# Kernel tuning notes

Measured on AMD Instinct MI355X. Metric: run time of the kernel, lower is better.

## Reference

```python
import jax, jax.numpy as jnp
import numpy as np

B, CIN, COUT, N = 64, 1024, 1024, 49   # batch, in_features, out_features, flattened spatial
GROUPS = 1
CHUNK = 16                              # output-channel tile to bound intermediate memory


def setup_inputs() -> dict:
    key = jax.random.key(0)
    k1, k2 = jax.random.split(key)
    x = jax.random.normal(k1, (B, CIN, N), dtype=jnp.float32)
    weight = jax.random.normal(k2, (COUT, CIN // GROUPS), dtype=jnp.float32)  # std=1.0 init
    bias = jnp.zeros((COUT,), dtype=jnp.float32)
    return {"x": x, "weight": weight, "bias": bias}


def norm_dist_inf(x, weight, groups, chunk):
    # x: [B, Cin, N], weight: [Cout, Cin//groups]
    # out[b, o, n] = max_d |x[b, g(o)*d + d', n] - weight[o, d']|  (L-inf distance)
    Bb, Cin, Nn = x.shape
    Cout, d = weight.shape
    og = Cout // groups
    xg = x.reshape(Bb, groups, d, Nn)                 # [B, g, d, N]
    wg = weight.reshape(groups, og, d)                # [g, og, d]
    # tile output channels to avoid materializing [B, Cout, Cin, N]
    wchunks = wg.reshape(groups, og // chunk, chunk, d).transpose(1, 0, 2, 3)  # [nc, g, chunk, d]

    def body(carry, wc):
        # diff: [B, g, chunk, d, N] -> max over d
        out = jnp.max(jnp.abs(xg[:, :, None, :, :] - wc[None, :, :, :, None]), axis=3)
        return carry, out                              # [B, g, chunk, N]

    _, outs = jax.lax.scan(body, None, wchunks)        # [nc, B, g, chunk, N]
    out = outs.transpose(1, 2, 0, 3, 4).reshape(Bb, Cout, Nn)
    return out


def reference(x, weight, bias):
    out = norm_dist_inf(x, weight, GROUPS, CHUNK)      # [B, Cout, N]
    return out + bias[None, :, None]
```

## Files before the change

### kernel.cpp

```cpp
#include <hip/hip_runtime.h>


constexpr int CIN  = 1024;
constexpr int COUT = 1024;
constexpr int NN   = 49;
constexpr int BB   = 64;
constexpr int P    = BB * NN;
constexpr int CPW  = 8;
constexpr int WPB  = 4;
constexpr int CPB  = CPW * WPB;
constexpr int KU   = 8;

__global__ __launch_bounds__(256) void ndist_kernel(
    const float* __restrict__ x, const float* __restrict__ w,
    const float* __restrict__ bias, float* __restrict__ out)
{
    const int lane = threadIdx.x & 63;
    const int wid  = __builtin_amdgcn_readfirstlane(threadIdx.x >> 6);

    const int p = blockIdx.x * BB + lane;
    const int b = p / NN;
    const int n = p - b * NN;
    const int o0 = blockIdx.y * CPB + wid * CPW;

    const float* __restrict__ xrow = x + (size_t)b * CIN * NN + n;

    float acc[CPW];
#pragma unroll
    for (int c = 0; c < CPW; ++c) acc[c] = 0.0f;

    for (int k0 = 0; k0 < CIN; k0 += KU) {
        float xv[KU];
#pragma unroll
        for (int j = 0; j < KU; ++j) xv[j] = xrow[(k0 + j) * NN];

#pragma unroll
        for (int c = 0; c < CPW; ++c) {
            const float* __restrict__ wr = w + (size_t)(o0 + c) * CIN + k0;
#pragma unroll
            for (int j = 0; j < KU; j += 2) {
                float d0 = xv[j]     - wr[j];
                float d1 = xv[j + 1] - wr[j + 1];
                acc[c] = fmaxf(fmaxf(acc[c], __builtin_fabsf(d0)),
                               __builtin_fabsf(d1));
            }
        }
    }

#pragma unroll
    for (int c = 0; c < CPW; ++c) {
        const int o = o0 + c;
        out[((size_t)b * COUT + o) * NN + n] = acc[c] + bias[o];
    }
}

extern "C" void kernel_launch(void* const* d_in, const int* in_sizes, int n_in,
                              void* d_out, int out_size, void* d_ws, size_t ws_size,
                              hipStream_t stream) {
    const float* x    = (const float*)d_in[0];
    const float* w    = (const float*)d_in[1];
    const float* bias = (const float*)d_in[2];
    float* out        = (float*)d_out;

    dim3 grid(P / BB, COUT / CPB);
    ndist_kernel<<<grid, 256, 0, stream>>>(x, w, bias, out);
}
```

Measured before the change: 150.8 us.

## Repack weights and use packed f32 subtract with max3 for L-inf distance

Adds a pre-pass that reorders weights into a k-tile by channel-group layout, so each wave reads a contiguous scalar block of 8 channels by 4 k values. The inner loop uses inline-asm v_pk_add_f32 with an SGPR weight operand to compute two channel differences per instruction, and v_max3_f32 with abs modifiers to fold two differences into the accumulator. It also double-buffers the x loads across k-tiles. This cuts VALU instruction count per element, at the cost of an extra 4 MB weight repack kernel on every call and a dependence on workspace size, with a fallback path when the workspace is too small.

```diff
diff --git a/kernel.cpp b/kernel.cpp
--- a/kernel.cpp
+++ b/kernel.cpp
@@ -1,5 +1,7 @@
 #include <hip/hip_runtime.h>
 
+
+typedef float v2f __attribute__((ext_vector_type(2)));
 
 constexpr int CIN  = 1024;
 constexpr int COUT = 1024;
@@ -9,10 +11,43 @@
 constexpr int CPW  = 8;
 constexpr int WPB  = 4;
 constexpr int CPB  = CPW * WPB;
-constexpr int KU   = 8;
+constexpr int KU   = 4;
+constexpr int NKT  = CIN / KU;
+
+__global__ void pack_w_kernel(const float* __restrict__ w, float* __restrict__ wq) {
+    int idx = blockIdx.x * 256 + threadIdx.x;
+    int o = idx >> 10, k = idx & 1023;
+    int kt = k >> 2, ku = k & 3, og = o >> 3, oc = o & 7;
+    wq[(((size_t)kt * (COUT / 8) + og) * KU + ku) * 8 + oc] = w[idx];
+}
+
+__device__ __forceinline__ void compute4(const float (&xv)[KU],
+                                         const v2f* __restrict__ wrow,
+                                         float (&acc)[CPW]) {
+    v2f wv[16];
+#pragma unroll
+    for (int q = 0; q < 16; ++q) wv[q] = wrow[q];
+#pragma unroll
+    for (int k = 0; k < KU; k += 2) {
+        v2f xx0 = { xv[k],     xv[k]     };
+        v2f xx1 = { xv[k + 1], xv[k + 1] };
+#pragma unroll
+        for (int cp = 0; cp < 4; ++cp) {
+            v2f d0, d1;
+            asm("v_pk_add_f32 %0, %1, %2 neg_lo:[0,1] neg_hi:[0,1]"
+                : "=v"(d0) : "s"(wv[k * 4 + cp]), "v"(xx0));
+            asm("v_pk_add_f32 %0, %1, %2 neg_lo:[0,1] neg_hi:[0,1]"
+                : "=v"(d1) : "s"(wv[(k + 1) * 4 + cp]), "v"(xx1));
+            asm("v_max3_f32 %0, %0, |%1|, |%2|"
+                : "+v"(acc[2 * cp])     : "v"(d0.x), "v"(d1.x));
+            asm("v_max3_f32 %0, %0, |%1|, |%2|"
+                : "+v"(acc[2 * cp + 1]) : "v"(d0.y), "v"(d1.y));
+        }
+    }
+}
 
 __global__ __launch_bounds__(256) void ndist_kernel(
-    const float* __restrict__ x, const float* __restrict__ w,
+    const float* __restrict__ x, const float* __restrict__ wq,
     const float* __restrict__ bias, float* __restrict__ out)
 {
     const int lane = threadIdx.x & 63;
@@ -21,32 +56,70 @@
     const int p = blockIdx.x * BB + lane;
     const int b = p / NN;
     const int n = p - b * NN;
+    const int og = blockIdx.y * WPB + wid;
+    const int o0 = og * CPW;
+
+    const float* __restrict__ xrow  = x + (size_t)b * CIN * NN + n;
+    const v2f*   __restrict__ wbase = (const v2f*)(wq + (size_t)og * 32);
+    constexpr size_t WKT = (size_t)(COUT / 8) * 16;
+
+    float acc[CPW];
+#pragma unroll
+    for (int c = 0; c < CPW; ++c) acc[c] = 0.0f;
+
+    float xa[KU], xb[KU];
+#pragma unroll
+    for (int j = 0; j < KU; ++j) xa[j] = xrow[j * NN];
+
+    for (int kt = 0; kt < NKT; kt += 2) {
+#pragma unroll
+        for (int j = 0; j < KU; ++j) xb[j] = xrow[((kt + 1) * KU + j) * NN];
+        compute4(xa, wbase + (size_t)kt * WKT, acc);
+
+        const int ktn = (kt + 2 < NKT) ? kt + 2 : 0;
+#pragma unroll
+        for (int j = 0; j < KU; ++j) xa[j] = xrow[(ktn * KU + j) * NN];
+        compute4(xb, wbase + (size_t)(kt + 1) * WKT, acc);
+    }
+
+#pragma unroll
+    for (int c = 0; c < CPW; ++c) {
+        const int o = o0 + c;
+        out[((size_t)b * COUT + o) * NN + n] = acc[c] + bias[o];
+    }
+}
+
+__global__ __launch_bounds__(256) void ndist_fallback(
+    const float* __restrict__ x, const float* __restrict__ w,
+    const float* __restrict__ bias, float* __restrict__ out)
+{
+    const int lane = threadIdx.x & 63;
+    const int wid  = __builtin_amdgcn_readfirstlane(threadIdx.x >> 6);
+    const int p = blockIdx.x * BB + lane;
+    const int b = p / NN, n = p - b * NN;
     const int o0 = blockIdx.y * CPB + wid * CPW;
-
     const float* __restrict__ xrow = x + (size_t)b * CIN * NN + n;
 
     float acc[CPW];
 #pragma unroll
     for (int c = 0; c < CPW; ++c) acc[c] = 0.0f;
 
-    for (int k0 = 0; k0 < CIN; k0 += KU) {
-        float xv[KU];
+    for (int k0 = 0; k0 < CIN; k0 += 8) {
+        float xv[8];
 #pragma unroll
-        for (int j = 0; j < KU; ++j) xv[j] = xrow[(k0 + j) * NN];
-
+        for (int j = 0; j < 8; ++j) xv[j] = xrow[(k0 + j) * NN];
 #pragma unroll
         for (int c = 0; c < CPW; ++c) {
             const float* __restrict__ wr = w + (size_t)(o0 + c) * CIN + k0;
 #pragma unroll
-            for (int j = 0; j < KU; j += 2) {
-                float d0 = xv[j]     - wr[j];
+            for (int j = 0; j < 8; j += 2) {
+                float d0 = xv[j] - wr[j];
                 float d1 = xv[j + 1] - wr[j + 1];
                 acc[c] = fmaxf(fmaxf(acc[c], __builtin_fabsf(d0)),
                                __builtin_fabsf(d1));
             }
         }
     }
-
 #pragma unroll
     for (int c = 0; c < CPW; ++c) {
         const int o = o0 + c;
@@ -62,6 +135,14 @@
     const float* bias = (const float*)d_in[2];
     float* out        = (float*)d_out;
 
-    dim3 grid(P / BB, COUT / CPB);
-    ndist_kernel<<<grid, 256, 0, stream>>>(x, w, bias, out);
+    const size_t wq_bytes = (size_t)COUT * CIN * sizeof(float);
+    if (ws_size >= wq_bytes) {
+        float* wq = (float*)d_ws;
+        pack_w_kernel<<<(COUT * CIN) / 256, 256, 0, stream>>>(w, wq);
+        dim3 grid(P / BB, COUT / CPB);
+        ndist_kernel<<<grid, 256, 0, stream>>>(x, wq, bias, out);
+    } else {
+        dim3 grid(P / BB, COUT / CPB);
+        ndist_fallback<<<grid, 256, 0, stream>>>(x, w, bias, out);
+    }
 }
```

After: 158.0 us. 4.7% more time.

## Double-buffer scalar weight loads and use packed subtract with max3 in inline asm

Applied to the files above, without the earlier changes.

Rewrites the L-inf distance kernel as single-wave blocks that each cover 8 output channels and 128 pixels (2 per lane). Weights are fetched with s_load_dwordx4 into SGPRs and x values into registers, double-buffered so the next tile's loads are issued before the current tile is computed. The inner loop uses v_pk_add_f32 with negation to subtract two elements at once and v_max3_f32 with abs modifiers to cut VALU instruction count. The gains in x reuse and instruction throughput come at the cost of hand-written asm, manual lgkmcnt waits, and a different grid shape and occupancy.

```diff
diff --git a/kernel.cpp b/kernel.cpp
--- a/kernel.cpp
+++ b/kernel.cpp
@@ -1,56 +1,131 @@
 #include <hip/hip_runtime.h>
 
+
+typedef float v2f  __attribute__((ext_vector_type(2)));
+typedef float v4sf __attribute__((ext_vector_type(4)));
 
 constexpr int CIN  = 1024;
 constexpr int COUT = 1024;
 constexpr int NN   = 49;
-constexpr int BB   = 64;
-constexpr int P    = BB * NN;
+constexpr int P    = 3136;
 constexpr int CPW  = 8;
-constexpr int WPB  = 4;
-constexpr int CPB  = CPW * WPB;
-constexpr int KU   = 8;
+constexpr int PIX  = 2;
+constexpr int PT   = 64 * PIX;
+constexpr int NPT  = (P + PT - 1) / PT;
+constexpr int NTL  = CIN / 4;
 
-__global__ __launch_bounds__(256) void ndist_kernel(
+#define PKSUB(d, wp, xp) \
+    asm("v_pk_add_f32 %0, %1, %2 neg_lo:[0,1] neg_hi:[0,1]" \
+        : "=v"(d) : "s"(wp), "v"(xp))
+#define AMAX3(a, lo, hi) \
+    asm("v_max3_f32 %0, %0, |%1|, |%2|" : "+v"(a) : "v"(lo), "v"(hi))
+
+#define ISSUE_W(buf, ptr) do {                                               \
+    asm volatile("s_load_dwordx4 %0, %1, 0x0"    : "=s"(buf[0]) : "s"(ptr)); \
+    asm volatile("s_load_dwordx4 %0, %1, 0x1000" : "=s"(buf[1]) : "s"(ptr)); \
+    asm volatile("s_load_dwordx4 %0, %1, 0x2000" : "=s"(buf[2]) : "s"(ptr)); \
+    asm volatile("s_load_dwordx4 %0, %1, 0x3000" : "=s"(buf[3]) : "s"(ptr)); \
+    asm volatile("s_load_dwordx4 %0, %1, 0x4000" : "=s"(buf[4]) : "s"(ptr)); \
+    asm volatile("s_load_dwordx4 %0, %1, 0x5000" : "=s"(buf[5]) : "s"(ptr)); \
+    asm volatile("s_load_dwordx4 %0, %1, 0x6000" : "=s"(buf[6]) : "s"(ptr)); \
+    asm volatile("s_load_dwordx4 %0, %1, 0x7000" : "=s"(buf[7]) : "s"(ptr)); \
+} while (0)
+
+#define SDRAIN() asm volatile("s_waitcnt lgkmcnt(0)" ::: "memory")
+
+__global__ __launch_bounds__(64) void ndist_kernel(
     const float* __restrict__ x, const float* __restrict__ w,
     const float* __restrict__ bias, float* __restrict__ out)
 {
-    const int lane = threadIdx.x & 63;
-    const int wid  = __builtin_amdgcn_readfirstlane(threadIdx.x >> 6);
+    const int lane  = threadIdx.x;
+    const int o0    = blockIdx.x * CPW;
+    const int pbase = blockIdx.y * PT;
 
-    const int p = blockIdx.x * BB + lane;
-    const int b = p / NN;
-    const int n = p - b * NN;
-    const int o0 = blockIdx.y * CPB + wid * CPW;
+    int bb[PIX], nn_[PIX];
+    const float* xp[PIX];
+#pragma unroll
+    for (int i = 0; i < PIX; ++i) {
+        const bool valid = (pbase + i * 64) < P;
+        const int  pi    = (valid ? pbase + i * 64 : pbase) + lane;
+        bb[i]  = pi / NN;
+        nn_[i] = pi - bb[i] * NN;
+        xp[i]  = x + (size_t)bb[i] * (CIN * NN) + nn_[i];
+    }
 
-    const float* __restrict__ xrow = x + (size_t)b * CIN * NN + n;
+    const float* wb = w + (size_t)o0 * CIN;
 
-    float acc[CPW];
+    float acc[CPW][PIX];
 #pragma unroll
-    for (int c = 0; c < CPW; ++c) acc[c] = 0.0f;
+    for (int c = 0; c < CPW; ++c)
+#pragma unroll
+        for (int i = 0; i < PIX; ++i) acc[c][i] = 0.0f;
 
-    for (int k0 = 0; k0 < CIN; k0 += KU) {
-        float xv[KU];
-#pragma unroll
-        for (int j = 0; j < KU; ++j) xv[j] = xrow[(k0 + j) * NN];
+    v2f  xA[PIX][2], xB[PIX][2];
+    v4sf wS0[8], wS1[8];
 
-#pragma unroll
-        for (int c = 0; c < CPW; ++c) {
-            const float* __restrict__ wr = w + (size_t)(o0 + c) * CIN + k0;
-#pragma unroll
-            for (int j = 0; j < KU; j += 2) {
-                float d0 = xv[j]     - wr[j];
-                float d1 = xv[j + 1] - wr[j + 1];
-                acc[c] = fmaxf(fmaxf(acc[c], __builtin_fabsf(d0)),
-                               __builtin_fabsf(d1));
-            }
-        }
+#define LOAD_X(dst, kt) do {                                   \
+        _Pragma("unroll")                                      \
+        for (int i = 0; i < PIX; ++i) {                        \
+            float a0 = xp[i][((kt) * 4 + 0) * NN];             \
+            float a1 = xp[i][((kt) * 4 + 1) * NN];             \
+            float a2 = xp[i][((kt) * 4 + 2) * NN];             \
+            float a3 = xp[i][((kt) * 4 + 3) * NN];             \
+            dst[i][0] = (v2f){a0, a1};                         \
+            dst[i][1] = (v2f){a2, a3};                         \
+        }                                                      \
+    } while (0)
+
+#define COMPUTE(xv, wbuf) do {                                 \
+        _Pragma("unroll")                                      \
+        for (int c = 0; c < CPW; ++c) {                        \
+            v2f wlo = __builtin_shufflevector(wbuf[c], wbuf[c], 0, 1); \
+            v2f whi = __builtin_shufflevector(wbuf[c], wbuf[c], 2, 3); \
+            _Pragma("unroll")                                  \
+            for (int i = 0; i < PIX; ++i) {                    \
+                v2f d0, d1;                                    \
+                PKSUB(d0, wlo, xv[i][0]);                      \
+                PKSUB(d1, whi, xv[i][1]);                      \
+                AMAX3(acc[c][i], d0.x, d0.y);                  \
+                AMAX3(acc[c][i], d1.x, d1.y);                  \
+            }                                                  \
+        }                                                      \
+    } while (0)
+
+    ISSUE_W(wS0, wb);
+    LOAD_X(xA, 0);
+    SDRAIN();
+
+    for (int kt = 0; kt < NTL - 2; kt += 2) {
+        const float* w1 = wb + (size_t)(kt + 1) * 4;
+        ISSUE_W(wS1, w1);
+        LOAD_X(xB, kt + 1);
+        COMPUTE(xA, wS0);
+        SDRAIN();
+
+        const float* w2 = wb + (size_t)(kt + 2) * 4;
+        ISSUE_W(wS0, w2);
+        LOAD_X(xA, kt + 2);
+        COMPUTE(xB, wS1);
+        SDRAIN();
+    }
+    {
+        const float* w1 = wb + (size_t)(NTL - 1) * 4;
+        ISSUE_W(wS1, w1);
+        LOAD_X(xB, NTL - 1);
+        COMPUTE(xA, wS0);
+        SDRAIN();
+        COMPUTE(xB, wS1);
     }
 
 #pragma unroll
-    for (int c = 0; c < CPW; ++c) {
-        const int o = o0 + c;
-        out[((size_t)b * COUT + o) * NN + n] = acc[c] + bias[o];
+    for (int i = 0; i < PIX; ++i) {
+        if ((pbase + i * 64) < P) {
+#pragma unroll
+            for (int c = 0; c < CPW; ++c) {
+                const int o = o0 + c;
+                out[((size_t)bb[i] * COUT + o) * NN + nn_[i]] = acc[c][i] + bias[o];
+            }
+        }
     }
 }
 
@@ -62,6 +137,6 @@
     const float* bias = (const float*)d_in[2];
     float* out        = (float*)d_out;
 
-    dim3 grid(P / BB, COUT / CPB);
-    ndist_kernel<<<grid, 256, 0, stream>>>(x, w, bias, out);
+    dim3 grid(COUT / CPW, NPT);
+    ndist_kernel<<<grid, 64, 0, stream>>>(x, w, bias, out);
 }
```

Result: slower. 154.5 us (+2.4%).

## Pack inputs to fp16 pairs and compute L-inf distance with packed half math

Applied to the files above, without the earlier changes.

Adds pre-kernels that convert weights and activations to packed fp16 pairs, with activations re-laid out per 64-position tile. The main kernel then tracks separate packed max and min of differences, avoiding abs and processing two channels per instruction. This cuts ALU work and memory traffic but adds two pack launches and loses precision relative to fp32. It keeps an fp32 fallback for when workspace is too small.

```diff
diff --git a/kernel.cpp b/kernel.cpp
--- a/kernel.cpp
+++ b/kernel.cpp
@@ -1,52 +1,115 @@
 #include <hip/hip_runtime.h>
 
+
+typedef _Float16 h2 __attribute__((ext_vector_type(2)));
 
 constexpr int CIN  = 1024;
 constexpr int COUT = 1024;
 constexpr int NN   = 49;
-constexpr int BB   = 64;
-constexpr int P    = BB * NN;
+constexpr int P    = 3136;
+constexpr int KP   = CIN / 2;
 constexpr int CPW  = 8;
-constexpr int WPB  = 4;
+constexpr int WPB  = 2;
 constexpr int CPB  = CPW * WPB;
 constexpr int KU   = 8;
+constexpr int NST  = KP / KU;
 
-__global__ __launch_bounds__(256) void ndist_kernel(
+__global__ void pack_w(const float* __restrict__ w, h2* __restrict__ wh) {
+    int idx = blockIdx.x * 256 + threadIdx.x;
+    int o = idx >> 9, kp = idx & (KP - 1);
+    const float* s = w + (size_t)o * CIN + 2 * kp;
+    wh[(size_t)o * KP + kp] = h2{(_Float16)s[0], (_Float16)s[1]};
+}
+
+__global__ void pack_x(const float* __restrict__ x, h2* __restrict__ xh) {
+    const int pp = threadIdx.x & 63, kk = threadIdx.x >> 6;
+    const int p  = blockIdx.x * 64 + pp;
+    const int kp = blockIdx.y * 4 + kk;
+    const int b = p / NN, n = p - b * NN;
+    const float* s = x + (size_t)b * (CIN * NN) + (size_t)(2 * kp) * NN + n;
+    xh[((size_t)blockIdx.x * KP + kp) * 64 + pp] = h2{(_Float16)s[0], (_Float16)s[NN]};
+}
+
+__global__ __launch_bounds__(128) void ndist_kernel(
+    const h2* __restrict__ xh, const h2* __restrict__ wh,
+    const float* __restrict__ bias, float* __restrict__ out)
+{
+    const int lane = threadIdx.x & 63;
+    const int wid  = __builtin_amdgcn_readfirstlane(threadIdx.x >> 6);
+
+    const int pt = blockIdx.y;
+    const int p  = pt * 64 + lane;
+    const int b  = p / NN, n = p - b * NN;
+    const int o0 = blockIdx.x * CPB + wid * CPW;
+
+    const h2* __restrict__ xp = xh + (size_t)pt * KP * 64 + lane;
+    const h2* __restrict__ wb = wh + (size_t)o0 * KP;
+
+    h2 accP[CPW], accN[CPW];
+#pragma unroll
+    for (int c = 0; c < CPW; ++c) {
+        accP[c] = h2{(_Float16)0.f, (_Float16)0.f};
+        accN[c] = h2{(_Float16)0.f, (_Float16)0.f};
+    }
+
+    for (int st = 0; st < NST; ++st) {
+        h2 xv[KU];
+#pragma unroll
+        for (int j = 0; j < KU; ++j) xv[j] = xp[(size_t)(st * KU + j) * 64];
+
+#pragma unroll
+        for (int c = 0; c < CPW; ++c) {
+            const h2* __restrict__ wr = wb + (size_t)c * KP + st * KU;
+#pragma unroll
+            for (int j = 0; j < KU; ++j) {
+                h2 d = xv[j] - wr[j];
+                accP[c] = __builtin_elementwise_max(accP[c], d);
+                accN[c] = __builtin_elementwise_min(accN[c], d);
+            }
+        }
+    }
+
+#pragma unroll
+    for (int c = 0; c < CPW; ++c) {
+        const int o = o0 + c;
+        float m = fmaxf(fmaxf((float)accP[c].x, (float)accP[c].y),
+                        fmaxf(-(float)accN[c].x, -(float)accN[c].y));
+        out[((size_t)b * COUT + o) * NN + n] = m + bias[o];
+    }
+}
+
+__global__ __launch_bounds__(128) void ndist_fallback(
     const float* __restrict__ x, const float* __restrict__ w,
     const float* __restrict__ bias, float* __restrict__ out)
 {
     const int lane = threadIdx.x & 63;
     const int wid  = __builtin_amdgcn_readfirstlane(threadIdx.x >> 6);
-
-    const int p = blockIdx.x * BB + lane;
-    const int b = p / NN;
-    const int n = p - b * NN;
-    const int o0 = blockIdx.y * CPB + wid * CPW;
-
+    const int p = blockIdx.y * 64 + lane;
+    const int b = p / NN, n = p - b * NN;
+    const int o0 = blockIdx.x * CPB + wid * CPW;
     const float* __restrict__ xrow = x + (size_t)b * CIN * NN + n;
+    const float* __restrict__ wb   = w + (size_t)o0 * CIN;
 
     float acc[CPW];
 #pragma unroll
     for (int c = 0; c < CPW; ++c) acc[c] = 0.0f;
 
-    for (int k0 = 0; k0 < CIN; k0 += KU) {
-        float xv[KU];
+    for (int k0 = 0; k0 < CIN; k0 += 8) {
+        float xv[8];
 #pragma unroll
-        for (int j = 0; j < KU; ++j) xv[j] = xrow[(k0 + j) * NN];
-
+        for (int j = 0; j < 8; ++j) xv[j] = xrow[(k0 + j) * NN];
 #pragma unroll
         for (int c = 0; c < CPW; ++c) {
-            const float* __restrict__ wr = w + (size_t)(o0 + c) * CIN + k0;
+            const float* __restrict__ wr = wb + (size_t)c * CIN + k0;
 #pragma unroll
-            for (int j = 0; j < KU; j += 2) {
-                float d0 = xv[j]     - wr[j];
+            for (int j = 0; j < 8; j += 2) {
+                float d0 = xv[j] - wr[j];
                 float d1 = xv[j + 1] - wr[j + 1];
                 acc[c] = fmaxf(fmaxf(acc[c], __builtin_fabsf(d0)),
                                __builtin_fabsf(d1));
             }
         }
     }
-
 #pragma unroll
     for (int c = 0; c < CPW; ++c) {
         const int o = o0 + c;
@@ -62,6 +125,16 @@
     const float* bias = (const float*)d_in[2];
     float* out        = (float*)d_out;
 
-    dim3 grid(P / BB, COUT / CPB);
-    ndist_kernel<<<grid, 256, 0, stream>>>(x, w, bias, out);
+    const size_t wh_bytes = (size_t)COUT * KP * sizeof(h2);
+    const size_t xh_bytes = (size_t)49 * KP * 64 * sizeof(h2);
+
+    if (ws_size >= wh_bytes + xh_bytes) {
+        h2* wh = (h2*)d_ws;
+        h2* xh = (h2*)((char*)d_ws + wh_bytes);
+        pack_w<<<(COUT * KP) / 256, 256, 0, stream>>>(w, wh);
+        pack_x<<<dim3(49, KP / 4), 256, 0, stream>>>(x, xh);
+        ndist_kernel<<<dim3(COUT / CPB, 49), 128, 0, stream>>>(xh, wh, bias, out);
+    } else {
+        ndist_fallback<<<dim3(COUT / CPB, 49), 128, 0, stream>>>(x, w, bias, out);
+    }
 }
```

New measurement: 189.3 us. 1.26x slower.
